# Kernel optimization log

Measured on AMD Instinct MI355X. Metric: run time of the kernel, lower is better.

## Reference

```python
import jax, jax.numpy as jnp
import numpy as np

B, T, C = 4, 2048, 1024
HEAD = 2048

def setup_inputs() -> dict:
    key = jax.random.key(0)
    ks = jax.random.split(key, 7)
    s = 1.0 / np.sqrt(C)
    return {
        "x":  jax.random.normal(ks[0], (B, T, C), dtype=jnp.float32),
        "Wq": jax.random.uniform(ks[1], (C, HEAD), dtype=jnp.float32, minval=-s, maxval=s),
        "bq": jax.random.uniform(ks[2], (HEAD,), dtype=jnp.float32, minval=-s, maxval=s),
        "Wk": jax.random.uniform(ks[3], (C, HEAD), dtype=jnp.float32, minval=-s, maxval=s),
        "bk": jax.random.uniform(ks[4], (HEAD,), dtype=jnp.float32, minval=-s, maxval=s),
        "Wv": jax.random.uniform(ks[5], (C, HEAD), dtype=jnp.float32, minval=-s, maxval=s),
        "bv": jax.random.uniform(ks[6], (HEAD,), dtype=jnp.float32, minval=-s, maxval=s),
    }

def reference(x, Wq, bq, Wk, bk, Wv, bv):
    # q,k,v: [B,T,HEAD]
    q = jnp.einsum('btc,ch->bth', x, Wq) + bq
    k = jnp.einsum('btc,ch->bth', x, Wk) + bk
    v = jnp.einsum('btc,ch->bth', x, Wv) + bv
    scale = x.shape[-1] ** -0.5  # NOTE: original scales by n_embed**-0.5, not head_size
    wei = jnp.einsum('bth,bsh->bts', q, k) * scale  # [B,T,T]
    Tn = x.shape[1]
    causal = jnp.tril(jnp.ones((Tn, Tn), dtype=bool))
    wei = jnp.where(causal, wei, -jnp.inf)
    wei = jax.nn.softmax(wei, axis=-1)
    # dropout is identity in eval mode
    out = jnp.einsum('bts,bsh->bth', wei, v)  # [B,T,HEAD]
    return out
```

## Files before the change

### kernel.cpp

```cpp
#include <hip/hip_runtime.h>


#define T_    2048
#define C_    1024
#define B_    4
#define NQK   4096
#define SCALE 0.03125f

typedef __attribute__((ext_vector_type(4))) float floatx4;
typedef __attribute__((ext_vector_type(8))) short short8;
typedef __attribute__((ext_vector_type(8))) unsigned short ushortx8;

__device__ __forceinline__ unsigned short f2bf(float f) {
  unsigned int u = __float_as_uint(f);
  unsigned int r = (u + 0x7fffu + ((u >> 16) & 1u)) >> 16;
  return (unsigned short)r;
}

__global__ void cast_x_kernel(const float* __restrict__ x, ushort* __restrict__ xbf) {
  int i = blockIdx.x * 256 + threadIdx.x;
  float4 v = ((const float4*)x)[i];
  ushort4 o;
  o.x = f2bf(v.x); o.y = f2bf(v.y); o.z = f2bf(v.z); o.w = f2bf(v.w);
  ((ushort4*)xbf)[i] = o;
}

__global__ void wcast_t_kernel(const float* __restrict__ Wq, const float* __restrict__ Wk,
                               const float* __restrict__ Wv, ushort* __restrict__ WtT) {
  int k0 = blockIdx.x * 32;
  int n0 = blockIdx.y * 32;
  const float* W = (n0 < 2048) ? Wq : (n0 < 4096 ? Wk : Wv);
  int nl0 = n0 & 2047;
  __shared__ ushort tile[32][33];
  int tx = threadIdx.x, ty = threadIdx.y;
  for (int r = ty; r < 32; r += 8)
    tile[r][tx] = f2bf(W[(size_t)(k0 + r) * 2048 + nl0 + tx]);
  __syncthreads();
  for (int r = ty; r < 32; r += 8)
    WtT[(size_t)(n0 + r) * 1024 + k0 + tx] = tile[tx][r];
}

__global__ void bias_cat_kernel(const float* __restrict__ bq, const float* __restrict__ bk,
                                const float* __restrict__ bv, float* __restrict__ bcat) {
  int i = blockIdx.x * 256 + threadIdx.x;
  if (i < 6144) {
    const float* s = (i < 2048) ? bq : (i < 4096 ? bk : bv);
    bcat[i] = s[i & 2047];
  }
}


#define MFMA16(a, b, c) __builtin_amdgcn_mfma_f32_16x16x32_bf16((a), (b), (c), 0, 0, 0)

#define GLDS16(gsrc, ldst)                                                                       \
  __builtin_amdgcn_global_load_lds((const __attribute__((address_space(1))) unsigned int*)(gsrc), \
                                   (__attribute__((address_space(3))) unsigned int*)(ldst), 16, 0, 0)

template <int LD>
__device__ __forceinline__ void stage_half(const ushort* gsrc, char* ldst) {
  GLDS16(gsrc, ldst);
  GLDS16(gsrc + 8 * LD, ldst + 1024);
}

#define BARX() do {                                        \
  __builtin_amdgcn_sched_barrier(0);                       \
  __builtin_amdgcn_s_barrier();                            \
  __builtin_amdgcn_sched_barrier(0);                       \
} while (0)

template <int LDA, int LDB>
__device__ __forceinline__ void prologue256(const ushort* Ap, const ushort* Bp,
                                            char* lds, int wave, int srcOffA, int srcOffB) {
  stage_half<LDA>(Ap + srcOffA,                     lds + wave * 2048);
  stage_half<LDA>(Ap + 128 * LDA + srcOffA,         lds + 16384 + wave * 2048);
  stage_half<LDB>(Bp + srcOffB,                     lds + 65536 + wave * 2048);
  stage_half<LDB>(Bp + 128 * LDB + srcOffB,         lds + 81920 + wave * 2048);
  stage_half<LDB>(Bp + 64 + srcOffB,                lds + 98304 + wave * 2048);
  stage_half<LDB>(Bp + 64 + 128 * LDB + srcOffB,    lds + 114688 + wave * 2048);
  __builtin_amdgcn_sched_barrier(0);
  asm volatile("s_waitcnt vmcnt(4)" ::: "memory");
  BARX();
}

template <int LDA, int LDB, bool TAIL>
__device__ __forceinline__ void iter256(const ushort* __restrict__ Ap,
                                        const ushort* __restrict__ Bp,
                                        char* lds, int kt0, int wave, int wm, int wn,
                                        int srcOffA, int srcOffB, int lnoff0,
                                        floatx4 (&acc)[8][4]) {
  char* rA0 = lds + wm * 16384;
  char* rA1 = rA0 + 32768;
  char* rB0 = lds + 65536 + (wn >> 1) * 16384 + (wn & 1) * 8192;
  char* rB1 = rB0 + 32768;
  const ushort* sA1 = Ap + (kt0 + 1) * 64 + srcOffA;
  const ushort* sA2 = Ap + (kt0 + 2) * 64 + srcOffA;
  const ushort* sB2 = Bp + (kt0 + 2) * 64 + srcOffB;
  const ushort* sB3 = Bp + (kt0 + 3) * 64 + srcOffB;
  const int lnoff1 = lnoff0 ^ 64;
  short8 af[4][2], b4[4][2];

#pragma unroll
  for (int mi = 0; mi < 4; ++mi) {
    af[mi][0] = *(const short8*)(rA0 + mi * 2048 + lnoff0);
    af[mi][1] = *(const short8*)(rA0 + mi * 2048 + lnoff1);
  }
#pragma unroll
  for (int nj = 0; nj < 4; ++nj) {
    b4[nj][0] = *(const short8*)(rB0 + nj * 2048 + lnoff0);
    b4[nj][1] = *(const short8*)(rB0 + nj * 2048 + lnoff1);
  }
  stage_half<LDA>(sA1, lds + 32768 + wave * 2048);
  stage_half<LDA>(sA1 + 128 * LDA, lds + 49152 + wave * 2048);
  __builtin_amdgcn_s_setprio(1);
#pragma unroll
  for (int mi = 0; mi < 4; ++mi)
#pragma unroll
    for (int nj = 0; nj < 4; ++nj) {
      acc[mi][nj] = MFMA16(af[mi][0], b4[nj][0], acc[mi][nj]);
      acc[mi][nj] = MFMA16(af[mi][1], b4[nj][1], acc[mi][nj]);
    }
  __builtin_amdgcn_s_setprio(0);
  BARX();

#pragma unroll
  for (int mi = 0; mi < 4; ++mi) {
    af[mi][0] = *(const short8*)(rA0 + (4 + mi) * 2048 + lnoff0);
    af[mi][1] = *(const short8*)(rA0 + (4 + mi) * 2048 + lnoff1);
  }
  if constexpr (!TAIL) {
    stage_half<LDB>(sB2, lds + 65536 + wave * 2048);
    stage_half<LDB>(sB2 + 128 * LDB, lds + 81920 + wave * 2048);
  }
  __builtin_amdgcn_s_setprio(1);
#pragma unroll
  for (int mi = 0; mi < 4; ++mi)
#pragma unroll
    for (int nj = 0; nj < 4; ++nj) {
      acc[4 + mi][nj] = MFMA16(af[mi][0], b4[nj][0], acc[4 + mi][nj]);
      acc[4 + mi][nj] = MFMA16(af[mi][1], b4[nj][1], acc[4 + mi][nj]);
    }
  __builtin_amdgcn_s_setprio(0);
  __builtin_amdgcn_sched_barrier(0);
  if constexpr (TAIL) asm volatile("s_waitcnt vmcnt(0)" ::: "memory");
  else                asm volatile("s_waitcnt vmcnt(4)" ::: "memory");
  BARX();

#pragma unroll
  for (int mi = 0; mi < 4; ++mi) {
    af[mi][0] = *(const short8*)(rA1 + mi * 2048 + lnoff0);
    af[mi][1] = *(const short8*)(rA1 + mi * 2048 + lnoff1);
  }
#pragma unroll
  for (int nj = 0; nj < 4; ++nj) {
    b4[nj][0] = *(const short8*)(rB1 + nj * 2048 + lnoff0);
    b4[nj][1] = *(const short8*)(rB1 + nj * 2048 + lnoff1);
  }
  if constexpr (!TAIL) {
    stage_half<LDA>(sA2, lds + wave * 2048);
    stage_half<LDA>(sA2 + 128 * LDA, lds + 16384 + wave * 2048);
  }
  __builtin_amdgcn_s_setprio(1);
#pragma unroll
  for (int mi = 0; mi < 4; ++mi)
#pragma unroll
    for (int nj = 0; nj < 4; ++nj) {
      acc[mi][nj] = MFMA16(af[mi][0], b4[nj][0], acc[mi][nj]);
      acc[mi][nj] = MFMA16(af[mi][1], b4[nj][1], acc[mi][nj]);
    }
  __builtin_amdgcn_s_setprio(0);
  BARX();

#pragma unroll
  for (int mi = 0; mi < 4; ++mi) {
    af[mi][0] = *(const short8*)(rA1 + (4 + mi) * 2048 + lnoff0);
    af[mi][1] = *(const short8*)(rA1 + (4 + mi) * 2048 + lnoff1);
  }
  if constexpr (!TAIL) {
    stage_half<LDB>(sB3, lds + 98304 + wave * 2048);
    stage_half<LDB>(sB3 + 128 * LDB, lds + 114688 + wave * 2048);
  }
  __builtin_amdgcn_s_setprio(1);
#pragma unroll
  for (int mi = 0; mi < 4; ++mi)
#pragma unroll
    for (int nj = 0; nj < 4; ++nj) {
      acc[4 + mi][nj] = MFMA16(af[mi][0], b4[nj][0], acc[4 + mi][nj]);
      acc[4 + mi][nj] = MFMA16(af[mi][1], b4[nj][1], acc[4 + mi][nj]);
    }
  __builtin_amdgcn_s_setprio(0);
  __builtin_amdgcn_sched_barrier(0);
  if constexpr (!TAIL) asm volatile("s_waitcnt vmcnt(4)" ::: "memory");
  BARX();
}

struct Addr256 {
  int wave, wm, wn, ln, ln15, lnoff0;
};
__device__ __forceinline__ Addr256 addr256() {
  Addr256 a;
  int tid = threadIdx.x;
  a.wave = tid >> 6; a.ln = tid & 63;
  a.wm = a.wave >> 2; a.wn = a.wave & 3;
  a.ln15 = a.ln & 15;
  a.lnoff0 = a.ln15 * 128 + (((a.ln >> 4) * 16) ^ ((a.ln15 & 7) << 4));
  return a;
}
template <int LD>
__device__ __forceinline__ int srcOff256(int wave, int ln) {
  return (wave * 16 + (ln >> 3)) * LD + (((ln & 7) * 8) ^ ((ln >> 3) << 3));
}

__global__ __launch_bounds__(512) void gemm_qk256(const ushort* __restrict__ xbf,
                                                  const ushort* __restrict__ WtT,
                                                  const float* __restrict__ bcat,
                                                  ushort* __restrict__ QK) {
  __shared__ __align__(16) char lds[131072];
  int tm = blockIdx.x, tn = blockIdx.y;
  Addr256 a = addr256();
  int srcOff = srcOff256<1024>(a.wave, a.ln);
  const ushort* Ap = xbf + (size_t)tm * 256 * 1024;
  const ushort* Bp = WtT + (size_t)tn * 256 * 1024;
  floatx4 acc[8][4];
#pragma unroll
  for (int i = 0; i < 8; ++i)
#pragma unroll
    for (int j = 0; j < 4; ++j) acc[i][j] = (floatx4){0.f, 0.f, 0.f, 0.f};

  prologue256<1024, 1024>(Ap, Bp, lds, a.wave, srcOff, srcOff);
#pragma unroll 1
  for (int i = 0; i < 7; ++i)
    iter256<1024, 1024, false>(Ap, Bp, lds, 2 * i, a.wave, a.wm, a.wn, srcOff, srcOff, a.lnoff0, acc);
  iter256<1024, 1024, true>(Ap, Bp, lds, 14, a.wave, a.wm, a.wn, srcOff, srcOff, a.lnoff0, acc);

  int colb = a.ln15, rowq = (a.ln >> 4) * 4;
  int colbase = tn * 256 + a.wn * 64 + colb;
  float bias[4];
#pragma unroll
  for (int nj = 0; nj < 4; ++nj) bias[nj] = bcat[colbase + nj * 16];
#pragma unroll
  for (int mi = 0; mi < 8; ++mi) {
    int row = tm * 256 + a.wm * 128 + mi * 16 + rowq;
#pragma unroll
    for (int r = 0; r < 4; ++r) {
      ushort* qrow = QK + (size_t)(row + r) * NQK;
#pragma unroll
      for (int nj = 0; nj < 4; ++nj)
        qrow[colbase + nj * 16] = f2bf(acc[mi][nj][r] + bias[nj]);
    }
  }
}

__global__ __launch_bounds__(512) void gemm_sv(const ushort* __restrict__ QK,
                                               const ushort* __restrict__ xbf,
                                               const ushort* __restrict__ WtT,
                                               const float* __restrict__ bcat,
                                               float* __restrict__ S,
                                               ushort* __restrict__ Vt) {
  __shared__ __align__(16) char lds[131072];
  int l = blockIdx.x;
  Addr256 a = addr256();
  floatx4 acc[8][4];
#pragma unroll
  for (int i = 0; i < 8; ++i)
#pragma unroll
    for (int j = 0; j < 4; ++j) acc[i][j] = (floatx4){0.f, 0.f, 0.f, 0.f};

  if (l < 144) {
    int t = l % 36, b = l / 36;
    int tm = (int)((sqrtf(8.f * t + 1.f) - 1.f) * 0.5f);
    while ((tm + 1) * (tm + 2) / 2 <= t) ++tm;
    while (tm * (tm + 1) / 2 > t) --tm;
    int tn = t - tm * (tm + 1) / 2;
    int srcOff = srcOff256<NQK>(a.wave, a.ln);
    const ushort* Ap = QK + (size_t)b * T_ * NQK + (size_t)tm * 256 * NQK;
    const ushort* Bp = QK + (size_t)b * T_ * NQK + (size_t)tn * 256 * NQK + 2048;
    prologue256<NQK, NQK>(Ap, Bp, lds, a.wave, srcOff, srcOff);
#pragma unroll 1
    for (int i = 0; i < 15; ++i)
      iter256<NQK, NQK, false>(Ap, Bp, lds, 2 * i, a.wave, a.wm, a.wn, srcOff, srcOff, a.lnoff0, acc);
    iter256<NQK, NQK, true>(Ap, Bp, lds, 30, a.wave, a.wm, a.wn, srcOff, srcOff, a.lnoff0, acc);

    float* Sb = S + (size_t)b * T_ * T_;
    int colb = a.ln15, rowq = (a.ln >> 4) * 4;
    int colbase = tn * 256 + a.wn * 64 + colb;
#pragma unroll
    for (int mi = 0; mi < 8; ++mi) {
      int row = tm * 256 + a.wm * 128 + mi * 16 + rowq;
#pragma unroll
      for (int r = 0; r < 4; ++r) {
        float* srow = Sb + (size_t)(row + r) * T_;
#pragma unroll
        for (int nj = 0; nj < 4; ++nj)
          srow[colbase + nj * 16] = acc[mi][nj][r] * SCALE;
      }
    }
  } else {
    int v = l - 144;
    int tn = v & 7, tmv = v >> 3;
    int srcOff = srcOff256<1024>(a.wave, a.ln);
    const ushort* Ap = xbf + (size_t)tmv * 256 * 1024;
    const ushort* Bp = WtT + (size_t)(4096 + tn * 256) * 1024;
    prologue256<1024, 1024>(Ap, Bp, lds, a.wave, srcOff, srcOff);
#pragma unroll 1
    for (int i = 0; i < 7; ++i)
      iter256<1024, 1024, false>(Ap, Bp, lds, 2 * i, a.wave, a.wm, a.wn, srcOff, srcOff, a.lnoff0, acc);
    iter256<1024, 1024, true>(Ap, Bp, lds, 14, a.wave, a.wm, a.wn, srcOff, srcOff, a.lnoff0, acc);

#pragma unroll
    for (int nj = 0; nj < 4; ++nj) {
      int h = a.wn * 64 + nj * 16 + a.ln15;
      float bv = bcat[4096 + tn * 256 + h];
      int xr = (h & 31) << 4;
#pragma unroll
      for (int mi = 0; mi < 8; ++mi) {
        int s0 = a.wm * 128 + mi * 16 + (a.ln >> 4) * 4;
        ushort4 o4;
        o4.x = f2bf(acc[mi][nj][0] + bv);
        o4.y = f2bf(acc[mi][nj][1] + bv);
        o4.z = f2bf(acc[mi][nj][2] + bv);
        o4.w = f2bf(acc[mi][nj][3] + bv);
        *(ushort4*)(lds + h * 512 + ((s0 * 2) ^ xr)) = o4;
      }
    }
    __syncthreads();
    int tid = threadIdx.x;
    int b = tmv >> 3, sbase = (tmv & 7) * 256;
    int hr = tid >> 5;
    int sc16 = tid & 31;
#pragma unroll
    for (int it = 0; it < 16; ++it) {
      int h = it * 16 + hr;
      ushortx8 vv = *(const ushortx8*)(lds + h * 512 + ((sc16 * 16) ^ ((h & 31) << 4)));
      *(ushortx8*)(Vt + ((size_t)b * T_ + tn * 256 + h) * T_ + sbase + sc16 * 8) = vv;
    }
  }
}

__global__ __launch_bounds__(512) void gemm_o256(const ushort* __restrict__ P,
                                                 const ushort* __restrict__ Vt,
                                                 float* __restrict__ O) {
  int tn = blockIdx.x, tm = 7 - blockIdx.y, b = blockIdx.z;
  __shared__ __align__(16) char lds[131072];
  Addr256 a = addr256();
  int srcOff = srcOff256<T_>(a.wave, a.ln);
  const ushort* Ap = P + (size_t)b * T_ * T_ + (size_t)tm * 256 * T_;
  const ushort* Bp = Vt + (size_t)b * T_ * T_ + (size_t)tn * 256 * T_;
  floatx4 acc[8][4];
#pragma unroll
  for (int i = 0; i < 8; ++i)
#pragma unroll
    for (int j = 0; j < 4; ++j) acc[i][j] = (floatx4){0.f, 0.f, 0.f, 0.f};

  int niter = (tm + 1) * 2;
  prologue256<T_, T_>(Ap, Bp, lds, a.wave, srcOff, srcOff);
#pragma unroll 1
  for (int i = 0; i < niter - 1; ++i)
    iter256<T_, T_, false>(Ap, Bp, lds, 2 * i, a.wave, a.wm, a.wn, srcOff, srcOff, a.lnoff0, acc);
  iter256<T_, T_, true>(Ap, Bp, lds, 2 * (niter - 1), a.wave, a.wm, a.wn, srcOff, srcOff, a.lnoff0, acc);

  float* Ob = O + (size_t)b * T_ * T_;
  int colb = a.ln15, rowq = (a.ln >> 4) * 4;
  int colbase = tn * 256 + a.wn * 64 + colb;
#pragma unroll
  for (int mi = 0; mi < 8; ++mi) {
    int row = tm * 256 + a.wm * 128 + mi * 16 + rowq;
#pragma unroll
    for (int r = 0; r < 4; ++r) {
      float* orow = Ob + (size_t)(row + r) * T_;
#pragma unroll
      for (int nj = 0; nj < 4; ++nj)
        orow[colbase + nj * 16] = acc[mi][nj][r];
    }
  }
}

__global__ __launch_bounds__(256) void softmax_causal(const float* __restrict__ S,
                                                      ushort* __restrict__ P) {
  int t = blockIdx.x, b = blockIdx.y;
  int tid = threadIdx.x;
  const float* srow = S + ((size_t)b * T_ + t) * T_;
  ushort* prow = P + ((size_t)b * T_ + t) * T_;
  int band = ((t >> 8) + 1) << 8;
  float xv[8];
  float m = -INFINITY;
#pragma unroll
  for (int c = 0; c < 2; ++c) {
    int s0 = c * 1024 + tid * 4;
    float* xs = xv + c * 4;
    if (s0 < band) {
      float4 v = *(const float4*)(srow + s0);
      xs[0] = (s0 + 0 <= t) ? v.x : -INFINITY;
      xs[1] = (s0 + 1 <= t) ? v.y : -INFINITY;
      xs[2] = (s0 + 2 <= t) ? v.z : -INFINITY;
      xs[3] = (s0 + 3 <= t) ? v.w : -INFINITY;
      m = fmaxf(fmaxf(fmaxf(xs[0], xs[1]), fmaxf(xs[2], xs[3])), m);
    } else {
      xs[0] = xs[1] = xs[2] = xs[3] = -INFINITY;
    }
  }
  __shared__ float sm4[4];
  int wid = tid >> 6, ln = tid & 63;
#pragma unroll
  for (int o = 32; o; o >>= 1) m = fmaxf(m, __shfl_xor(m, o));
  if (ln == 0) sm4[wid] = m;
  __syncthreads();
  m = fmaxf(fmaxf(sm4[0], sm4[1]), fmaxf(sm4[2], sm4[3]));
  __syncthreads();
  float sum = 0.f;
#pragma unroll
  for (int k = 0; k < 8; ++k) { xv[k] = __expf(xv[k] - m); sum += xv[k]; }
#pragma unroll
  for (int o = 32; o; o >>= 1) sum += __shfl_xor(sum, o);
  if (ln == 0) sm4[wid] = sum;
  __syncthreads();
  sum = sm4[0] + sm4[1] + sm4[2] + sm4[3];
  float inv = 1.0f / sum;
#pragma unroll
  for (int c = 0; c < 2; ++c) {
    int s0 = c * 1024 + tid * 4;
    if (s0 < band) {
      ushort4 o4;
      o4.x = f2bf(xv[c * 4 + 0] * inv);
      o4.y = f2bf(xv[c * 4 + 1] * inv);
      o4.z = f2bf(xv[c * 4 + 2] * inv);
      o4.w = f2bf(xv[c * 4 + 3] * inv);
      *(ushort4*)(prow + s0) = o4;
    }
  }
}

extern "C" void kernel_launch(void* const* d_in, const int* in_sizes, int n_in,
                              void* d_out, int out_size, void* d_ws, size_t ws_size,
                              hipStream_t stream) {
  (void)in_sizes; (void)n_in; (void)out_size; (void)ws_size;
  const float* x  = (const float*)d_in[0];
  const float* Wq = (const float*)d_in[1];
  const float* bq = (const float*)d_in[2];
  const float* Wk = (const float*)d_in[3];
  const float* bk = (const float*)d_in[4];
  const float* Wv = (const float*)d_in[5];
  const float* bv = (const float*)d_in[6];

  char* ws = (char*)d_ws;
  ushort* xbf  = (ushort*)(ws + 0);
  ushort* WtT  = (ushort*)(ws + 16777216);
  float*  bcat = (float*) (ws + 29360128);
  ushort* QK   = (ushort*)(ws + 29384704);
  ushort* P    = (ushort*)(ws + 96493568);
  ushort* Vt   = (ushort*)(ws + 130048000);

  float* S = (float*)d_out;
  float* O = (float*)d_out;

  cast_x_kernel  <<<8192, 256, 0, stream>>>(x, xbf);
  wcast_t_kernel <<<dim3(32, 192), dim3(32, 8), 0, stream>>>(Wq, Wk, Wv, WtT);
  bias_cat_kernel<<<24, 256, 0, stream>>>(bq, bk, bv, bcat);
  gemm_qk256     <<<dim3(32, 16), 512, 0, stream>>>(xbf, WtT, bcat, QK);
  gemm_sv        <<<400, 512, 0, stream>>>(QK, xbf, WtT, bcat, S, Vt);
  softmax_causal <<<dim3(2048, 4), 256, 0, stream>>>(S, P);
  gemm_o256      <<<dim3(8, 8, 4), 512, 0, stream>>>(P, Vt, O);
}
```

Baseline: 335.2 us.

## Fuse prep kernels, split-K balance PV GEMM with atomics, remap SV blocks per XCD

Merges the three preprocessing kernels into a single launch to cut launch overhead. Rebalances the causal P·V GEMM: the tall row-tiles (tm>=4) are split along K into two slots each, so each block does at most 8 iterations. The split results are accumulated with atomicAdd into O, which requires the softmax kernel to zero the S rows for t>=1024, since S aliases O. Also remaps gemm_sv block indices so each XCD handles one batch for better L2 locality. The cost is atomic traffic and ordering-dependent floating-point summation.

```diff
diff --git a/kernel.cpp b/kernel.cpp
--- a/kernel.cpp
+++ b/kernel.cpp
@@ -17,35 +17,36 @@
   return (unsigned short)r;
 }
 
-__global__ void cast_x_kernel(const float* __restrict__ x, ushort* __restrict__ xbf) {
-  int i = blockIdx.x * 256 + threadIdx.x;
-  float4 v = ((const float4*)x)[i];
-  ushort4 o;
-  o.x = f2bf(v.x); o.y = f2bf(v.y); o.z = f2bf(v.z); o.w = f2bf(v.w);
-  ((ushort4*)xbf)[i] = o;
-}
-
-__global__ void wcast_t_kernel(const float* __restrict__ Wq, const float* __restrict__ Wk,
-                               const float* __restrict__ Wv, ushort* __restrict__ WtT) {
-  int k0 = blockIdx.x * 32;
-  int n0 = blockIdx.y * 32;
-  const float* W = (n0 < 2048) ? Wq : (n0 < 4096 ? Wk : Wv);
-  int nl0 = n0 & 2047;
-  __shared__ ushort tile[32][33];
-  int tx = threadIdx.x, ty = threadIdx.y;
-  for (int r = ty; r < 32; r += 8)
-    tile[r][tx] = f2bf(W[(size_t)(k0 + r) * 2048 + nl0 + tx]);
-  __syncthreads();
-  for (int r = ty; r < 32; r += 8)
-    WtT[(size_t)(n0 + r) * 1024 + k0 + tx] = tile[tx][r];
-}
-
-__global__ void bias_cat_kernel(const float* __restrict__ bq, const float* __restrict__ bk,
-                                const float* __restrict__ bv, float* __restrict__ bcat) {
-  int i = blockIdx.x * 256 + threadIdx.x;
-  if (i < 6144) {
-    const float* s = (i < 2048) ? bq : (i < 4096 ? bk : bv);
-    bcat[i] = s[i & 2047];
+__global__ void prep_kernel(const float* __restrict__ x, ushort* __restrict__ xbf,
+                            const float* __restrict__ Wq, const float* __restrict__ Wk,
+                            const float* __restrict__ Wv, ushort* __restrict__ WtT,
+                            const float* __restrict__ bq, const float* __restrict__ bk,
+                            const float* __restrict__ bv, float* __restrict__ bcat) {
+  int bx = blockIdx.x, tid = threadIdx.x;
+  if (bx < 8192) {
+    int i = bx * 256 + tid;
+    float4 v = ((const float4*)x)[i];
+    ushort4 o;
+    o.x = f2bf(v.x); o.y = f2bf(v.y); o.z = f2bf(v.z); o.w = f2bf(v.w);
+    ((ushort4*)xbf)[i] = o;
+  } else if (bx < 8192 + 6144) {
+    int w = bx - 8192;
+    int k0 = (w & 31) * 32, n0 = (w >> 5) * 32;
+    const float* W = (n0 < 2048) ? Wq : (n0 < 4096 ? Wk : Wv);
+    int nl0 = n0 & 2047;
+    __shared__ ushort tile[32][33];
+    int tx = tid & 31, ty = tid >> 5;
+    for (int r = ty; r < 32; r += 8)
+      tile[r][tx] = f2bf(W[(size_t)(k0 + r) * 2048 + nl0 + tx]);
+    __syncthreads();
+    for (int r = ty; r < 32; r += 8)
+      WtT[(size_t)(n0 + r) * 1024 + k0 + tx] = tile[tx][r];
+  } else {
+    int i = (bx - 14336) * 256 + tid;
+    if (i < 6144) {
+      const float* s = (i < 2048) ? bq : (i < 4096 ? bk : bv);
+      bcat[i] = s[i & 2047];
+    }
   }
 }
 
@@ -266,7 +267,9 @@
     for (int j = 0; j < 4; ++j) acc[i][j] = (floatx4){0.f, 0.f, 0.f, 0.f};
 
   if (l < 144) {
-    int t = l % 36, b = l / 36;
+    int xcd = l & 7, j = l >> 3;
+    int b = xcd >> 1;
+    int t = (xcd & 1) * 18 + j;
     int tm = (int)((sqrtf(8.f * t + 1.f) - 1.f) * 0.5f);
     while ((tm + 1) * (tm + 2) / 2 <= t) ++tm;
     while (tm * (tm + 1) / 2 > t) --tm;
@@ -339,46 +342,63 @@
 __global__ __launch_bounds__(512) void gemm_o256(const ushort* __restrict__ P,
                                                  const ushort* __restrict__ Vt,
                                                  float* __restrict__ O) {
-  int tn = blockIdx.x, tm = 7 - blockIdx.y, b = blockIdx.z;
+  static constexpr int SLOT_TM[12] = {7, 7, 3, 6, 6, 5, 5, 2, 4, 4, 1, 0};
+  static constexpr int SLOT_I0[12] = {0, 8, 0, 0, 7, 0, 6, 0, 0, 5, 0, 0};
+  static constexpr int SLOT_NI[12] = {8, 8, 8, 7, 7, 6, 6, 6, 5, 5, 4, 2};
+  int tn = blockIdx.x, b = blockIdx.y, slot = blockIdx.z;
+  int tm = SLOT_TM[slot], i0 = SLOT_I0[slot], ni = SLOT_NI[slot];
   __shared__ __align__(16) char lds[131072];
   Addr256 a = addr256();
   int srcOff = srcOff256<T_>(a.wave, a.ln);
-  const ushort* Ap = P + (size_t)b * T_ * T_ + (size_t)tm * 256 * T_;
-  const ushort* Bp = Vt + (size_t)b * T_ * T_ + (size_t)tn * 256 * T_;
+  const ushort* Ap = P + (size_t)b * T_ * T_ + (size_t)tm * 256 * T_ + i0 * 128;
+  const ushort* Bp = Vt + (size_t)b * T_ * T_ + (size_t)tn * 256 * T_ + i0 * 128;
   floatx4 acc[8][4];
 #pragma unroll
   for (int i = 0; i < 8; ++i)
 #pragma unroll
     for (int j = 0; j < 4; ++j) acc[i][j] = (floatx4){0.f, 0.f, 0.f, 0.f};
 
-  int niter = (tm + 1) * 2;
   prologue256<T_, T_>(Ap, Bp, lds, a.wave, srcOff, srcOff);
 #pragma unroll 1
-  for (int i = 0; i < niter - 1; ++i)
+  for (int i = 0; i < ni - 1; ++i)
     iter256<T_, T_, false>(Ap, Bp, lds, 2 * i, a.wave, a.wm, a.wn, srcOff, srcOff, a.lnoff0, acc);
-  iter256<T_, T_, true>(Ap, Bp, lds, 2 * (niter - 1), a.wave, a.wm, a.wn, srcOff, srcOff, a.lnoff0, acc);
+  iter256<T_, T_, true>(Ap, Bp, lds, 2 * (ni - 1), a.wave, a.wm, a.wn, srcOff, srcOff, a.lnoff0, acc);
 
   float* Ob = O + (size_t)b * T_ * T_;
   int colb = a.ln15, rowq = (a.ln >> 4) * 4;
   int colbase = tn * 256 + a.wn * 64 + colb;
-#pragma unroll
-  for (int mi = 0; mi < 8; ++mi) {
-    int row = tm * 256 + a.wm * 128 + mi * 16 + rowq;
-#pragma unroll
-    for (int r = 0; r < 4; ++r) {
-      float* orow = Ob + (size_t)(row + r) * T_;
-#pragma unroll
-      for (int nj = 0; nj < 4; ++nj)
-        orow[colbase + nj * 16] = acc[mi][nj][r];
-    }
-  }
-}
-
-__global__ __launch_bounds__(256) void softmax_causal(const float* __restrict__ S,
+  if (tm >= 4) {
+#pragma unroll
+    for (int mi = 0; mi < 8; ++mi) {
+      int row = tm * 256 + a.wm * 128 + mi * 16 + rowq;
+#pragma unroll
+      for (int r = 0; r < 4; ++r) {
+        float* orow = Ob + (size_t)(row + r) * T_;
+#pragma unroll
+        for (int nj = 0; nj < 4; ++nj)
+          atomicAdd(&orow[colbase + nj * 16], acc[mi][nj][r]);
+      }
+    }
+  } else {
+#pragma unroll
+    for (int mi = 0; mi < 8; ++mi) {
+      int row = tm * 256 + a.wm * 128 + mi * 16 + rowq;
+#pragma unroll
+      for (int r = 0; r < 4; ++r) {
+        float* orow = Ob + (size_t)(row + r) * T_;
+#pragma unroll
+        for (int nj = 0; nj < 4; ++nj)
+          orow[colbase + nj * 16] = acc[mi][nj][r];
+      }
+    }
+  }
+}
+
+__global__ __launch_bounds__(256) void softmax_causal(float* __restrict__ S,
                                                       ushort* __restrict__ P) {
   int t = blockIdx.x, b = blockIdx.y;
   int tid = threadIdx.x;
-  const float* srow = S + ((size_t)b * T_ + t) * T_;
+  float* srow = S + ((size_t)b * T_ + t) * T_;
   ushort* prow = P + ((size_t)b * T_ + t) * T_;
   int band = ((t >> 8) + 1) << 8;
   float xv[8];
@@ -427,6 +447,11 @@
       *(ushort4*)(prow + s0) = o4;
     }
   }
+  if (t >= 1024) {
+    float4 z = {0.f, 0.f, 0.f, 0.f};
+    ((float4*)srow)[tid] = z;
+    ((float4*)srow)[256 + tid] = z;
+  }
 }
 
 extern "C" void kernel_launch(void* const* d_in, const int* in_sizes, int n_in,
@@ -452,11 +477,9 @@
   float* S = (float*)d_out;
   float* O = (float*)d_out;
 
-  cast_x_kernel  <<<8192, 256, 0, stream>>>(x, xbf);
-  wcast_t_kernel <<<dim3(32, 192), dim3(32, 8), 0, stream>>>(Wq, Wk, Wv, WtT);
-  bias_cat_kernel<<<24, 256, 0, stream>>>(bq, bk, bv, bcat);
+  prep_kernel    <<<14360, 256, 0, stream>>>(x, xbf, Wq, Wk, Wv, WtT, bq, bk, bv, bcat);
   gemm_qk256     <<<dim3(32, 16), 512, 0, stream>>>(xbf, WtT, bcat, QK);
   gemm_sv        <<<400, 512, 0, stream>>>(QK, xbf, WtT, bcat, S, Vt);
   softmax_causal <<<dim3(2048, 4), 256, 0, stream>>>(S, P);
-  gemm_o256      <<<dim3(8, 8, 4), 512, 0, stream>>>(P, Vt, O);
-}
+  gemm_o256      <<<dim3(8, 4, 12), 512, 0, stream>>>(P, Vt, O);
+}
```

Result: slower. 344.9 us (+2.9%).
